# Kernel optimization log

Hardware: AMD Instinct MI355X
Metric: run time of the kernel (lower is better)

The kernel has to match this reference:

```python
import jax, jax.numpy as jnp
import numpy as np

B, T, I, H, C = 4096, 64, 60, 60, 600


def setup_inputs() -> dict:
    key = jax.random.key(0)
    ks = jax.random.split(key, 7)
    s = 1.0 / np.sqrt(H).astype(np.float32)  # PyTorch RNN init bound
    u = lambda k, shape: jax.random.uniform(k, shape, jnp.float32, -s, s)
    return {
        "x": jax.random.normal(ks[0], (B, T, I), jnp.float32),
        "w_ih": u(ks[1], (2, 3 * H, I)),   # per-direction [3H, I], gates (r,z,n)
        "w_hh": u(ks[2], (2, 3 * H, H)),
        "b_ih": u(ks[3], (2, 3 * H)),
        "b_hh": u(ks[4], (2, 3 * H)),
        "fc_w": u(ks[5], (C, 2 * H * T)),
        "fc_b": u(ks[6], (C,)),
    }


def _gru_dir(x_tbi, w_ih, w_hh, b_ih, b_hh):
    # Precompute input-side gate pre-activations for all timesteps: [T, B, 3H]
    gx = jnp.einsum('tbi,gi->tbg', x_tbi, w_ih) + b_ih
    h0 = jnp.zeros((x_tbi.shape[1], H), x_tbi.dtype)

    def step(h, gx_t):
        gh = h @ w_hh.T + b_hh                      # [B, 3H]
        r = jax.nn.sigmoid(gx_t[:, :H] + gh[:, :H])
        z = jax.nn.sigmoid(gx_t[:, H:2 * H] + gh[:, H:2 * H])
        n = jnp.tanh(gx_t[:, 2 * H:] + r * gh[:, 2 * H:])
        h_new = (1.0 - z) * n + z * h
        return h_new, h_new

    _, hs = jax.lax.scan(step, h0, gx)
    return hs  # [T, B, H]


def reference(x, w_ih, w_hh, b_ih, b_hh, fc_w, fc_b):
    xt = jnp.swapaxes(x, 0, 1)                        # [T, B, I]
    fwd = _gru_dir(xt, w_ih[0], w_hh[0], b_ih[0], b_hh[0])           # [T,B,H]
    bwd = _gru_dir(xt[::-1], w_ih[1], w_hh[1], b_ih[1], b_hh[1])[::-1]
    out = jnp.concatenate([fwd, bwd], axis=-1)        # [T, B, 2H]
    out = jnp.swapaxes(out, 0, 1).reshape(x.shape[0], -1)  # [B, T*2H]
    return out @ fc_w.T + fc_b
```

## Files before the change

kernel.cpp:

```cpp
#include <hip/hip_runtime.h>

#define BB 4096
#define TT 64
#define NH 60
#define KF 7680
#define NC 600

typedef short bf16x8 __attribute__((ext_vector_type(8)));
typedef float f32x4 __attribute__((ext_vector_type(4)));
#define MFMA16(A,B,C) __builtin_amdgcn_mfma_f32_16x16x32_bf16(A,B,C,0,0,0)

__device__ __forceinline__ unsigned short f2bf(float v) {
    unsigned int u = __float_as_uint(v);
    return (unsigned short)((u + 0x7FFFu + ((u >> 16) & 1u)) >> 16);
}
__device__ __forceinline__ float bf2f(unsigned short b) {
    return __uint_as_float(((unsigned int)b) << 16);
}
__device__ __forceinline__ float sigf(float v)     { return 1.f / (1.f + __expf(-v)); }
__device__ __forceinline__ float tanhfast(float v) { return 2.f / (1.f + __expf(-2.f * v)) - 1.f; }

__global__ __launch_bounds__(512, 2) void gru4_kernel(
    const float* __restrict__ x,
    const float* __restrict__ w_ih,
    const float* __restrict__ w_hh,
    const float* __restrict__ b_ih,
    const float* __restrict__ b_hh,
    unsigned int* __restrict__ hs)
{
    __shared__ unsigned short XHh[2][32 * 128];
    __shared__ unsigned short XHl[2][32 * 128];
    __shared__ unsigned int hstage[2][32][60];

    const int tid = threadIdx.x;
    const int d  = blockIdx.y;
    const int b0 = blockIdx.x * 32;
    const int wave = tid >> 6, lane = tid & 63;
    const int mtile = wave >> 2, ug = wave & 3;
    const int l15 = lane & 15, lq = lane >> 4;
    const int j = ug * 16 + l15;
    const bool jv = j < NH;
    const int m = mtile * 16 + l15;
    const int rbase = mtile * 16 + lq * 4;

    for (int i = tid; i < 2 * 32 * 128; i += 512) { (&XHh[0][0])[i] = 0; (&XHl[0][0])[i] = 0; }

    bf16x8 wHf[3][4], wLf[3][4];
#pragma unroll
    for (int g = 0; g < 3; ++g) {
#pragma unroll
        for (int kt = 0; kt < 4; ++kt) {
            bf16x8 h8, l8;
            const int kb = kt * 32 + lq * 8;
#pragma unroll
            for (int e = 0; e < 8; ++e) {
                const int k = kb + e;
                float v = 0.f;
                if (jv) {
                    if (k < 60)                    v = w_ih[(size_t)d * 10800 + (g * 60 + j) * 60 + k];
                    else if (k >= 64 && k < 124)   v = w_hh[(size_t)d * 10800 + (g * 60 + j) * 60 + (k - 64)];
                }
                const unsigned short hb = f2bf(v);
                const unsigned short lb = f2bf(v - bf2f(hb));
                h8[e] = (short)hb; l8[e] = (short)lb;
            }
            wHf[g][kt] = h8; wLf[g][kt] = l8;
        }
    }

    float bir = 0, biz = 0, bin = 0, bhr = 0, bhz = 0, bhn = 0;
    if (jv) {
        bir = b_ih[d * 180 + j]; biz = b_ih[d * 180 + 60 + j]; bin = b_ih[d * 180 + 120 + j];
        bhr = b_hh[d * 180 + j]; bhz = b_hh[d * 180 + 60 + j]; bhn = b_hh[d * 180 + 120 + j];
    }

    const bool xact = tid < 480;
    const int rowx = xact ? tid / 15 : 31;
    const int cx   = xact ? tid % 15 : 14;
    const float* xb = x + ((size_t)(b0 + rowx) * TT) * 60 + cx * 4;
    unsigned int* hsb = hs + (size_t)(b0 + rowx) * KF + d * 60 + cx * 4;

    __syncthreads();

    if (xact) {
        const int tt0 = d ? (TT - 1) : 0;
        const float4 v = *(const float4*)(xb + tt0 * 60);
        const float vv[4] = {v.x, v.y, v.z, v.w};
#pragma unroll
        for (int e = 0; e < 4; ++e) {
            const int k = cx * 4 + e;
            const int idx = rowx * 128 + (((k >> 3) ^ (rowx & 7)) << 3) + (k & 7);
            const unsigned short hb = f2bf(vv[e]);
            XHh[0][idx] = hb; XHl[0][idx] = f2bf(vv[e] - bf2f(hb));
        }
    }
    float hold[4] = {0.f, 0.f, 0.f, 0.f};
    __syncthreads();

#pragma unroll 2
    for (int s = 0; s < TT; ++s) {
        const int p = s & 1, pn = p ^ 1;
        const int tt = d ? (TT - 1 - s) : s;

        float4 xp = make_float4(0.f, 0.f, 0.f, 0.f);
        const bool morex = (s < TT - 1) && xact;
        if (morex) xp = *(const float4*)(xb + (d ? (TT - 2 - s) : (s + 1)) * 60);

        f32x4 aR0 = {0,0,0,0}, aR1 = {0,0,0,0}, aZ0 = {0,0,0,0}, aZ1 = {0,0,0,0},
              aNX = {0,0,0,0}, aNH_ = {0,0,0,0};
        const unsigned short* Xh = &XHh[p][0];
        const unsigned short* Xl = &XHl[p][0];
#pragma unroll
        for (int kt = 0; kt < 4; ++kt) {
            const int c = kt * 4 + lq;
            const int off = m * 128 + ((c ^ (m & 7)) << 3);
            const bf16x8 aH = *(const bf16x8*)(Xh + off);
            const bf16x8 aL = *(const bf16x8*)(Xl + off);
            if (kt < 2) {
                aR0 = MFMA16(aH, wHf[0][kt], aR0); aR0 = MFMA16(aH, wLf[0][kt], aR0); aR0 = MFMA16(aL, wHf[0][kt], aR0);
                aZ0 = MFMA16(aH, wHf[1][kt], aZ0); aZ0 = MFMA16(aH, wLf[1][kt], aZ0); aZ0 = MFMA16(aL, wHf[1][kt], aZ0);
                aNX = MFMA16(aH, wHf[2][kt], aNX); aNX = MFMA16(aH, wLf[2][kt], aNX); aNX = MFMA16(aL, wHf[2][kt], aNX);
            } else {
                aR1 = MFMA16(aH, wHf[0][kt], aR1); aR1 = MFMA16(aH, wLf[0][kt], aR1); aR1 = MFMA16(aL, wHf[0][kt], aR1);
                aZ1 = MFMA16(aH, wHf[1][kt], aZ1); aZ1 = MFMA16(aH, wLf[1][kt], aZ1); aZ1 = MFMA16(aL, wHf[1][kt], aZ1);
                aNH_ = MFMA16(aH, wHf[2][kt], aNH_); aNH_ = MFMA16(aH, wLf[2][kt], aNH_); aNH_ = MFMA16(aL, wHf[2][kt], aNH_);
            }
        }

        float hnew[4];
#pragma unroll
        for (int r = 0; r < 4; ++r) {
            const float rr = sigf(aR0[r] + aR1[r] + bir + bhr);
            const float zz = sigf(aZ0[r] + aZ1[r] + biz + bhz);
            const float nn = tanhfast(aNX[r] + bin + rr * (aNH_[r] + bhn));
            hnew[r] = (1.f - zz) * nn + zz * hold[r];
            hold[r] = hnew[r];
        }

        if (jv) {
#pragma unroll
            for (int r = 0; r < 4; ++r) {
                const int rw = rbase + r;
                const int k = 64 + j;
                const int idx = rw * 128 + (((k >> 3) ^ (rw & 7)) << 3) + (k & 7);
                const unsigned short hb = f2bf(hnew[r]);
                const unsigned short lb = f2bf(hnew[r] - bf2f(hb));
                XHh[pn][idx] = hb; XHl[pn][idx] = lb;
                hstage[pn][rw][j] = ((unsigned int)hb << 16) | lb;
            }
        }
        if (morex) {
            const float vv[4] = {xp.x, xp.y, xp.z, xp.w};
#pragma unroll
            for (int e = 0; e < 4; ++e) {
                const int k = cx * 4 + e;
                const int idx = rowx * 128 + (((k >> 3) ^ (rowx & 7)) << 3) + (k & 7);
                const unsigned short hb = f2bf(vv[e]);
                XHh[pn][idx] = hb; XHl[pn][idx] = f2bf(vv[e] - bf2f(hb));
            }
        }
        __syncthreads();

        if (xact) {
            const uint4 hv = *(const uint4*)&hstage[pn][rowx][cx * 4];
            *(uint4*)(hsb + (size_t)tt * 120) = hv;
        }
    }
}

__global__ void out_init_kernel(const float* __restrict__ fcb, float* __restrict__ out) {
    const int i = blockIdx.x * 1024 + threadIdx.x;
    out[i] = fcb[i % NC];
}

__global__ __launch_bounds__(512, 2) void fc4_kernel(
    const unsigned int* __restrict__ hs,
    const float* __restrict__ fcw,
    float* __restrict__ out)
{
    __shared__ unsigned short Ash[2][256 * 64];
    __shared__ unsigned short Bsh[2][128 * 64];

    const int tid = threadIdx.x;
    const int m0 = blockIdx.x * 256;
    const int n0 = blockIdx.y * 128;
    const int k0 = blockIdx.z * 2560;
    const int wave = tid >> 6, lane = tid & 63;
    const int wm = wave >> 1, wn = wave & 1;
    const int l15 = lane & 15, lq = lane >> 4;

    f32x4 acc[4][4];
#pragma unroll
    for (int a = 0; a < 4; ++a)
#pragma unroll
        for (int b = 0; b < 4; ++b) acc[a][b] = (f32x4){0, 0, 0, 0};

    uint4 pa[4]; float4 pb[2];

#define STAGE_LOAD(t) do {                                                          \
    const int kc_ = k0 + (t) * 32;                                                  \
    _Pragma("unroll")                                                               \
    for (int it = 0; it < 4; ++it) {                                                \
        const int g_ = tid + it * 512, row_ = g_ >> 3, qi_ = g_ & 7;                \
        pa[it] = *(const uint4*)(hs + (size_t)(m0 + row_) * KF + kc_ + qi_ * 4);    \
    }                                                                               \
    _Pragma("unroll")                                                               \
    for (int it = 0; it < 2; ++it) {                                                \
        const int g_ = tid + it * 512, row_ = g_ >> 3, qi_ = g_ & 7;                \
        const int cc_ = n0 + row_;                                                  \
        pb[it] = (cc_ < NC) ? *(const float4*)(fcw + (size_t)cc_ * KF + kc_ + qi_ * 4) \
                            : make_float4(0.f, 0.f, 0.f, 0.f);                      \
    }                                                                               \
} while (0)

#define STAGE_WRITE(buf) do {                                                       \
    _Pragma("unroll")                                                               \
    for (int it = 0; it < 4; ++it) {                                                \
        const int g_ = tid + it * 512, row_ = g_ >> 3, qi_ = g_ & 7;                \
        const int ch_ = qi_ >> 1, hf_ = qi_ & 1;                                    \
        unsigned short* base_ = &Ash[buf][row_ * 64];                               \
        uint2 wh_, wl_;                                                             \
        wh_.x = (pa[it].x >> 16) | (pa[it].y & 0xFFFF0000u);                        \
        wh_.y = (pa[it].z >> 16) | (pa[it].w & 0xFFFF0000u);                        \
        wl_.x = (pa[it].x & 0xFFFFu) | (pa[it].y << 16);                            \
        wl_.y = (pa[it].z & 0xFFFFu) | (pa[it].w << 16);                            \
        *(uint2*)(base_ + ((ch_ ^ (row_ & 7)) << 3) + hf_ * 4) = wh_;               \
        *(uint2*)(base_ + (((ch_ | 4) ^ (row_ & 7)) << 3) + hf_ * 4) = wl_;         \
    }                                                                               \
    _Pragma("unroll")                                                               \
    for (int it = 0; it < 2; ++it) {                                                \
        const int g_ = tid + it * 512, row_ = g_ >> 3, qi_ = g_ & 7;                \
        const int ch_ = qi_ >> 1, hf_ = qi_ & 1;                                    \
        unsigned short* base_ = &Bsh[buf][row_ * 64];                               \
        const float bv_[4] = {pb[it].x, pb[it].y, pb[it].z, pb[it].w};              \
        unsigned short h4_[4], l4_[4];                                              \
        _Pragma("unroll")                                                           \
        for (int e = 0; e < 4; ++e) { h4_[e] = f2bf(bv_[e]); l4_[e] = f2bf(bv_[e] - bf2f(h4_[e])); } \
        uint2 wh_, wl_;                                                             \
        wh_.x = (unsigned int)h4_[0] | ((unsigned int)h4_[1] << 16);                \
        wh_.y = (unsigned int)h4_[2] | ((unsigned int)h4_[3] << 16);                \
        wl_.x = (unsigned int)l4_[0] | ((unsigned int)l4_[1] << 16);                \
        wl_.y = (unsigned int)l4_[2] | ((unsigned int)l4_[3] << 16);                \
        *(uint2*)(base_ + ((ch_ ^ (row_ & 7)) << 3) + hf_ * 4) = wh_;               \
        *(uint2*)(base_ + (((ch_ | 4) ^ (row_ & 7)) << 3) + hf_ * 4) = wl_;         \
    }                                                                               \
} while (0)

#define MFMA_PHASE(buf) do {                                                        \
    const unsigned short* Ab_ = &Ash[buf][0];                                       \
    const unsigned short* Bb_ = &Bsh[buf][0];                                       \
    bf16x8 aH_[4], aL_[4], bH_[4], bL_[4];                                          \
    _Pragma("unroll")                                                               \
    for (int t = 0; t < 4; ++t) {                                                   \
        const int mr_ = wm * 64 + t * 16 + l15;                                     \
        const unsigned short* p_ = Ab_ + mr_ * 64;                                  \
        aH_[t] = *(const bf16x8*)(p_ + ((lq ^ (mr_ & 7)) << 3));                    \
        aL_[t] = *(const bf16x8*)(p_ + (((lq | 4) ^ (mr_ & 7)) << 3));              \
        const int nr_ = wn * 64 + t * 16 + l15;                                     \
        const unsigned short* q_ = Bb_ + nr_ * 64;                                  \
        bH_[t] = *(const bf16x8*)(q_ + ((lq ^ (nr_ & 7)) << 3));                    \
        bL_[t] = *(const bf16x8*)(q_ + (((lq | 4) ^ (nr_ & 7)) << 3));              \
    }                                                                               \
    _Pragma("unroll")                                                               \
    for (int mt = 0; mt < 4; ++mt)                                                  \
        _Pragma("unroll")                                                           \
        for (int nt = 0; nt < 4; ++nt) {                                            \
            acc[mt][nt] = MFMA16(aH_[mt], bH_[nt], acc[mt][nt]);                    \
            acc[mt][nt] = MFMA16(aH_[mt], bL_[nt], acc[mt][nt]);                    \
            acc[mt][nt] = MFMA16(aL_[mt], bH_[nt], acc[mt][nt]);                    \
        }                                                                           \
} while (0)

#define BARRIER_LGKM() do {                                                         \
    asm volatile("s_waitcnt lgkmcnt(0)" ::: "memory");                              \
    __builtin_amdgcn_s_barrier();                                                   \
    __builtin_amdgcn_sched_barrier(0);                                              \
} while (0)

    STAGE_LOAD(0);
    STAGE_WRITE(0);
    STAGE_LOAD(1);
    __syncthreads();

#pragma unroll 1
    for (int t = 0; t < 80; t += 2) {
        STAGE_WRITE(1);
        if (t + 2 < 80) STAGE_LOAD(t + 2);
        MFMA_PHASE(0);
        BARRIER_LGKM();
        if (t + 2 < 80) STAGE_WRITE(0);
        if (t + 3 < 80) STAGE_LOAD(t + 3);
        MFMA_PHASE(1);
        BARRIER_LGKM();
    }

#pragma unroll
    for (int mt = 0; mt < 4; ++mt) {
        const int row = m0 + wm * 64 + mt * 16 + lq * 4;
#pragma unroll
        for (int nt = 0; nt < 4; ++nt) {
            const int col = n0 + wn * 64 + nt * 16 + l15;
            if (col < NC) {
#pragma unroll
                for (int r = 0; r < 4; ++r)
                    atomicAdd(out + (size_t)(row + r) * NC + col, acc[mt][nt][r]);
            }
        }
    }
#undef STAGE_LOAD
#undef STAGE_WRITE
#undef MFMA_PHASE
#undef BARRIER_LGKM
}

extern "C" void kernel_launch(void* const* d_in, const int* in_sizes, int n_in,
                              void* d_out, int out_size, void* d_ws, size_t ws_size,
                              hipStream_t stream) {
    (void)in_sizes; (void)n_in; (void)out_size;
    const float* x    = (const float*)d_in[0];
    const float* w_ih = (const float*)d_in[1];
    const float* w_hh = (const float*)d_in[2];
    const float* b_ih = (const float*)d_in[3];
    const float* b_hh = (const float*)d_in[4];
    const float* fcw  = (const float*)d_in[5];
    const float* fcb  = (const float*)d_in[6];
    float* out = (float*)d_out;
    unsigned int* hs = (unsigned int*)d_ws;

    if (ws_size < (size_t)KF * BB * sizeof(unsigned int)) return;

    out_init_kernel<<<dim3((BB * NC) / 1024), 1024, 0, stream>>>(fcb, out);
    gru4_kernel<<<dim3(BB / 32, 2), 512, 0, stream>>>(x, w_ih, w_hh, b_ih, b_hh, hs);
    fc4_kernel<<<dim3(BB / 256, 5, 3), 512, 0, stream>>>(hs, fcw, out);
}
```

Before: 365.6 us.

## Drop low-bf16 split of FC weights and restructure FC GEMM tiling

The FC GEMM now represents fc_w as a single bf16 instead of a hi/lo pair, cutting the MFMA count per tile from three to two. A is stored packed in LDS and unpacked into hi/lo at fragment-load time. Tiles move to 128x128 with 256 threads and 64-wide K chunks, split across two A buffers written by different thread halves. This lowers compute and LDS traffic, but loses precision on the weight side and changes the pipeline's synchronization pattern.

```diff
diff --git a/kernel.cpp b/kernel.cpp
--- a/kernel.cpp
+++ b/kernel.cpp
@@ -19,6 +19,20 @@
 }
 __device__ __forceinline__ float sigf(float v)     { return 1.f / (1.f + __expf(-v)); }
 __device__ __forceinline__ float tanhfast(float v) { return 2.f / (1.f + __expf(-2.f * v)) - 1.f; }
+
+__device__ __forceinline__ void unpk(const uint4 a, const uint4 b, bf16x8& hi, bf16x8& lo) {
+    uint4 h, l;
+    h.x = (a.x >> 16) | (a.y & 0xFFFF0000u);
+    h.y = (a.z >> 16) | (a.w & 0xFFFF0000u);
+    h.z = (b.x >> 16) | (b.y & 0xFFFF0000u);
+    h.w = (b.z >> 16) | (b.w & 0xFFFF0000u);
+    l.x = (a.x & 0xFFFFu) | (a.y << 16);
+    l.y = (a.z & 0xFFFFu) | (a.w << 16);
+    l.z = (b.x & 0xFFFFu) | (b.y << 16);
+    l.w = (b.z & 0xFFFFu) | (b.w << 16);
+    hi = __builtin_bit_cast(bf16x8, h);
+    lo = __builtin_bit_cast(bf16x8, l);
+}
 
 __global__ __launch_bounds__(512, 2) void gru4_kernel(
     const float* __restrict__ x,
@@ -173,125 +187,129 @@
     out[i] = fcb[i % NC];
 }
 
-__global__ __launch_bounds__(512, 2) void fc4_kernel(
+__global__ __launch_bounds__(256, 2) void fc6_kernel(
     const unsigned int* __restrict__ hs,
     const float* __restrict__ fcw,
     float* __restrict__ out)
 {
-    __shared__ unsigned short Ash[2][256 * 64];
-    __shared__ unsigned short Bsh[2][128 * 64];
+    __shared__ unsigned int  A0[128 * 32];
+    __shared__ unsigned int  A1[128 * 32];
+    __shared__ unsigned short Bsm[2][128 * 64];
 
     const int tid = threadIdx.x;
-    const int m0 = blockIdx.x * 256;
+    const int m0 = blockIdx.x * 128;
     const int n0 = blockIdx.y * 128;
     const int k0 = blockIdx.z * 2560;
     const int wave = tid >> 6, lane = tid & 63;
     const int wm = wave >> 1, wn = wave & 1;
     const int l15 = lane & 15, lq = lane >> 4;
 
+    const int srow = tid >> 4;
+    const int sc   = tid & 15;
+    const bool hA1 = sc >= 8;
+    const int ci   = sc & 7;
+
     f32x4 acc[4][4];
 #pragma unroll
     for (int a = 0; a < 4; ++a)
 #pragma unroll
         for (int b = 0; b < 4; ++b) acc[a][b] = (f32x4){0, 0, 0, 0};
 
-    uint4 pa[4]; float4 pb[2];
-
-#define STAGE_LOAD(t) do {                                                          \
-    const int kc_ = k0 + (t) * 32;                                                  \
-    _Pragma("unroll")                                                               \
-    for (int it = 0; it < 4; ++it) {                                                \
-        const int g_ = tid + it * 512, row_ = g_ >> 3, qi_ = g_ & 7;                \
-        pa[it] = *(const uint4*)(hs + (size_t)(m0 + row_) * KF + kc_ + qi_ * 4);    \
-    }                                                                               \
-    _Pragma("unroll")                                                               \
-    for (int it = 0; it < 2; ++it) {                                                \
-        const int g_ = tid + it * 512, row_ = g_ >> 3, qi_ = g_ & 7;                \
+    uint4 pa[8]; float4 pb[8];
+
+#define LOAD_A(kc_) do {                                                            \
+    _Pragma("unroll")                                                               \
+    for (int it = 0; it < 8; ++it) {                                                \
+        const int row_ = srow + it * 16;                                            \
+        pa[it] = *(const uint4*)(hs + (size_t)(m0 + row_) * KF + (kc_) + sc * 4);   \
+    }                                                                               \
+} while (0)
+
+#define WRITE_A(ap_) do {                                                           \
+    _Pragma("unroll")                                                               \
+    for (int it = 0; it < 8; ++it) {                                                \
+        const int row_ = srow + it * 16;                                            \
+        *(uint4*)((ap_) + row_ * 32 + ((ci ^ (row_ & 7)) << 2)) = pa[it];           \
+    }                                                                               \
+} while (0)
+
+#define LOAD_B(kc_) do {                                                            \
+    _Pragma("unroll")                                                               \
+    for (int it = 0; it < 8; ++it) {                                                \
+        const int row_ = srow + it * 16;                                            \
         const int cc_ = n0 + row_;                                                  \
-        pb[it] = (cc_ < NC) ? *(const float4*)(fcw + (size_t)cc_ * KF + kc_ + qi_ * 4) \
+        pb[it] = (cc_ < NC) ? *(const float4*)(fcw + (size_t)cc_ * KF + (kc_) + sc * 4) \
                             : make_float4(0.f, 0.f, 0.f, 0.f);                      \
     }                                                                               \
 } while (0)
 
-#define STAGE_WRITE(buf) do {                                                       \
-    _Pragma("unroll")                                                               \
-    for (int it = 0; it < 4; ++it) {                                                \
-        const int g_ = tid + it * 512, row_ = g_ >> 3, qi_ = g_ & 7;                \
-        const int ch_ = qi_ >> 1, hf_ = qi_ & 1;                                    \
-        unsigned short* base_ = &Ash[buf][row_ * 64];                               \
-        uint2 wh_, wl_;                                                             \
-        wh_.x = (pa[it].x >> 16) | (pa[it].y & 0xFFFF0000u);                        \
-        wh_.y = (pa[it].z >> 16) | (pa[it].w & 0xFFFF0000u);                        \
-        wl_.x = (pa[it].x & 0xFFFFu) | (pa[it].y << 16);                            \
-        wl_.y = (pa[it].z & 0xFFFFu) | (pa[it].w << 16);                            \
-        *(uint2*)(base_ + ((ch_ ^ (row_ & 7)) << 3) + hf_ * 4) = wh_;               \
-        *(uint2*)(base_ + (((ch_ | 4) ^ (row_ & 7)) << 3) + hf_ * 4) = wl_;         \
-    }                                                                               \
-    _Pragma("unroll")                                                               \
-    for (int it = 0; it < 2; ++it) {                                                \
-        const int g_ = tid + it * 512, row_ = g_ >> 3, qi_ = g_ & 7;                \
-        const int ch_ = qi_ >> 1, hf_ = qi_ & 1;                                    \
-        unsigned short* base_ = &Bsh[buf][row_ * 64];                               \
-        const float bv_[4] = {pb[it].x, pb[it].y, pb[it].z, pb[it].w};              \
-        unsigned short h4_[4], l4_[4];                                              \
+#define WRITE_B(bp_) do {                                                           \
+    _Pragma("unroll")                                                               \
+    for (int it = 0; it < 8; ++it) {                                                \
+        const int row_ = srow + it * 16;                                            \
+        const unsigned short h0_ = f2bf(pb[it].x), h1_ = f2bf(pb[it].y);            \
+        const unsigned short h2_ = f2bf(pb[it].z), h3_ = f2bf(pb[it].w);            \
+        uint2 wv_;                                                                  \
+        wv_.x = (unsigned int)h0_ | ((unsigned int)h1_ << 16);                      \
+        wv_.y = (unsigned int)h2_ | ((unsigned int)h3_ << 16);                      \
+        *(uint2*)((bp_) + row_ * 64 + (((sc >> 1) ^ (row_ & 7)) << 3) + (sc & 1) * 4) = wv_; \
+    }                                                                               \
+} while (0)
+
+#define MFMA_PH(ha_, bb_, kt_) do {                                                 \
+    bf16x8 aH_[4], aL_[4], bF_[4];                                                  \
+    _Pragma("unroll")                                                               \
+    for (int t_ = 0; t_ < 4; ++t_) {                                                \
+        const int mr_ = wm * 64 + t_ * 16 + l15;                                    \
+        const unsigned int* pr_ = (ha_) + mr_ * 32;                                 \
+        const uint4 c0_ = *(const uint4*)(pr_ + (((2 * lq) ^ (mr_ & 7)) << 2));     \
+        const uint4 c1_ = *(const uint4*)(pr_ + (((2 * lq + 1) ^ (mr_ & 7)) << 2)); \
+        unpk(c0_, c1_, aH_[t_], aL_[t_]);                                           \
+        const int nr_ = wn * 64 + t_ * 16 + l15;                                    \
+        bF_[t_] = *(const bf16x8*)((bb_) + nr_ * 64 + ((((kt_) * 4 + lq) ^ (nr_ & 7)) << 3)); \
+    }                                                                               \
+    _Pragma("unroll")                                                               \
+    for (int mt_ = 0; mt_ < 4; ++mt_)                                               \
         _Pragma("unroll")                                                           \
-        for (int e = 0; e < 4; ++e) { h4_[e] = f2bf(bv_[e]); l4_[e] = f2bf(bv_[e] - bf2f(h4_[e])); } \
-        uint2 wh_, wl_;                                                             \
-        wh_.x = (unsigned int)h4_[0] | ((unsigned int)h4_[1] << 16);                \
-        wh_.y = (unsigned int)h4_[2] | ((unsigned int)h4_[3] << 16);                \
-        wl_.x = (unsigned int)l4_[0] | ((unsigned int)l4_[1] << 16);                \
-        wl_.y = (unsigned int)l4_[2] | ((unsigned int)l4_[3] << 16);                \
-        *(uint2*)(base_ + ((ch_ ^ (row_ & 7)) << 3) + hf_ * 4) = wh_;               \
-        *(uint2*)(base_ + (((ch_ | 4) ^ (row_ & 7)) << 3) + hf_ * 4) = wl_;         \
-    }                                                                               \
-} while (0)
-
-#define MFMA_PHASE(buf) do {                                                        \
-    const unsigned short* Ab_ = &Ash[buf][0];                                       \
-    const unsigned short* Bb_ = &Bsh[buf][0];                                       \
-    bf16x8 aH_[4], aL_[4], bH_[4], bL_[4];                                          \
-    _Pragma("unroll")                                                               \
-    for (int t = 0; t < 4; ++t) {                                                   \
-        const int mr_ = wm * 64 + t * 16 + l15;                                     \
-        const unsigned short* p_ = Ab_ + mr_ * 64;                                  \
-        aH_[t] = *(const bf16x8*)(p_ + ((lq ^ (mr_ & 7)) << 3));                    \
-        aL_[t] = *(const bf16x8*)(p_ + (((lq | 4) ^ (mr_ & 7)) << 3));              \
-        const int nr_ = wn * 64 + t * 16 + l15;                                     \
-        const unsigned short* q_ = Bb_ + nr_ * 64;                                  \
-        bH_[t] = *(const bf16x8*)(q_ + ((lq ^ (nr_ & 7)) << 3));                    \
-        bL_[t] = *(const bf16x8*)(q_ + (((lq | 4) ^ (nr_ & 7)) << 3));              \
-    }                                                                               \
-    _Pragma("unroll")                                                               \
-    for (int mt = 0; mt < 4; ++mt)                                                  \
-        _Pragma("unroll")                                                           \
-        for (int nt = 0; nt < 4; ++nt) {                                            \
-            acc[mt][nt] = MFMA16(aH_[mt], bH_[nt], acc[mt][nt]);                    \
-            acc[mt][nt] = MFMA16(aH_[mt], bL_[nt], acc[mt][nt]);                    \
-            acc[mt][nt] = MFMA16(aL_[mt], bH_[nt], acc[mt][nt]);                    \
+        for (int nt_ = 0; nt_ < 4; ++nt_) {                                         \
+            acc[mt_][nt_] = MFMA16(aH_[mt_], bF_[nt_], acc[mt_][nt_]);              \
+            acc[mt_][nt_] = MFMA16(aL_[mt_], bF_[nt_], acc[mt_][nt_]);              \
         }                                                                           \
 } while (0)
 
-#define BARRIER_LGKM() do {                                                         \
+#define LGKM_BAR() do {                                                             \
     asm volatile("s_waitcnt lgkmcnt(0)" ::: "memory");                              \
     __builtin_amdgcn_s_barrier();                                                   \
     __builtin_amdgcn_sched_barrier(0);                                              \
 } while (0)
 
-    STAGE_LOAD(0);
-    STAGE_WRITE(0);
-    STAGE_LOAD(1);
-    __syncthreads();
+    LOAD_A(k0);
+    LOAD_B(k0);
+    if (!hA1) WRITE_A(A0);
+    WRITE_B(&Bsm[0][0]);
+    if (!hA1) LOAD_A(k0 + 64);
+    LOAD_B(k0 + 64);
+    LGKM_BAR();
 
 #pragma unroll 1
-    for (int t = 0; t < 80; t += 2) {
-        STAGE_WRITE(1);
-        if (t + 2 < 80) STAGE_LOAD(t + 2);
-        MFMA_PHASE(0);
-        BARRIER_LGKM();
-        if (t + 2 < 80) STAGE_WRITE(0);
-        if (t + 3 < 80) STAGE_LOAD(t + 3);
-        MFMA_PHASE(1);
-        BARRIER_LGKM();
+    for (int T = 0; T < 40; ++T) {
+        const int bm = T & 1;
+        const unsigned short* Bcur = &Bsm[bm][0];
+        unsigned short* Bnxt = &Bsm[bm ^ 1][0];
+        const int kc1 = k0 + (T + 1 < 40 ? T + 1 : 39) * 64;
+        const int kc2 = k0 + (T + 2 < 40 ? (T + 2 < 40 ? T + 2 : 39) : 39) * 64;
+
+        if (hA1) WRITE_A(A1);
+        if (hA1) LOAD_A(kc1);
+        MFMA_PH(A0, Bcur, 0);
+        LGKM_BAR();
+
+        if (!hA1) WRITE_A(A0);
+        WRITE_B(Bnxt);
+        if (!hA1) LOAD_A(kc2);
+        LOAD_B(kc2);
+        MFMA_PH(A1, Bcur, 1);
+        LGKM_BAR();
     }
 
 #pragma unroll
@@ -307,10 +325,12 @@
             }
         }
     }
-#undef STAGE_LOAD
-#undef STAGE_WRITE
-#undef MFMA_PHASE
-#undef BARRIER_LGKM
+#undef LOAD_A
+#undef WRITE_A
+#undef LOAD_B
+#undef WRITE_B
+#undef MFMA_PH
+#undef LGKM_BAR
 }
 
 extern "C" void kernel_launch(void* const* d_in, const int* in_sizes, int n_in,
@@ -331,5 +351,5 @@
 
     out_init_kernel<<<dim3((BB * NC) / 1024), 1024, 0, stream>>>(fcb, out);
     gru4_kernel<<<dim3(BB / 32, 2), 512, 0, stream>>>(x, w_ih, w_hh, b_ih, b_hh, hs);
-    fc4_kernel<<<dim3(BB / 256, 5, 3), 512, 0, stream>>>(hs, fcw, out);
-}
+    fc6_kernel<<<dim3(BB / 128, 5, 3), 256, 0, stream>>>(hs, fcw, out);
+}
```

New measurement: 691.4 us. 89.1% more time.
